# Performance work log

Measured on AMD Instinct MI355X. Metric: run time of the kernel, lower is better.

The kernel has to match this reference:

```python
import jax, jax.numpy as jnp
import numpy as np
from jax import lax

B, CIN, IMG, K = 128, 3, 112, 7
C = 1024      # hidden_channels * channel_dilation
HID = 512     # hidden_channels
HW = (IMG // K) ** 2  # 256 patches
EPS = 1e-5


def _prelu(x, a):
    return jnp.where(x > 0, x, a * x)


def _bn(x, g, b):
    # BatchNorm2d with track_running_stats=False: always uses batch stats
    m = x.mean(axis=(0, 2, 3), keepdims=True)
    v = x.var(axis=(0, 2, 3), keepdims=True)
    return (x - m) * lax.rsqrt(v + EPS) * g[None, :, None, None] + b[None, :, None, None]


def setup_inputs() -> dict:
    key = jax.random.key(0)
    ks = jax.random.split(key, 16)
    d = {
        'x':  jax.random.normal(ks[0], (B, CIN, IMG, IMG), jnp.float32),
        'w0': jax.random.normal(ks[1], (C, CIN, K, K), jnp.float32) * 0.05,
        'b0': jax.random.normal(ks[2], (C,), jnp.float32) * 0.01,
        'a0': jnp.full((1,), 0.25, jnp.float32),
    }
    for i in range(1, 4):
        kw, kb = jax.random.split(jax.random.fold_in(key, i))
        d[f'w{i}'] = jax.random.normal(kw, (C, C), jnp.float32) * 0.02
        d[f'b{i}'] = jax.random.normal(kb, (C,), jnp.float32) * 0.01
        d[f'g{i}'] = jnp.ones((C,), jnp.float32)
        d[f'bt{i}'] = jnp.zeros((C,), jnp.float32)
        d[f'p{i}'] = jnp.full((1,), 0.25, jnp.float32)
    d['pos'] = jax.random.normal(ks[3], (1, HW, C), jnp.float32)
    d['am'] = jnp.full((1,), 0.25, jnp.float32)
    d['wm'] = jax.random.normal(ks[4], (HID, C), jnp.float32) * 0.03
    d['bm'] = jax.random.normal(ks[5], (HID,), jnp.float32) * 0.01
    pkeys = jax.random.split(ks[6], B)
    d['perm'] = jax.vmap(lambda k: jax.random.permutation(k, HW))(pkeys).astype(jnp.int32)
    return d


def reference(x, w0, b0, a0,
              w1, b1, g1, bt1, p1,
              w2, b2, g2, bt2, p2,
              w3, b3, g3, bt3, p3,
              pos, am, wm, bm, perm):
    # patch-embed conv: stride = kernel_size -> [B, C, 16, 16]
    h = lax.conv_general_dilated(x, w0, (K, K), 'VALID',
                                 dimension_numbers=('NCHW', 'OIHW', 'NCHW'))
    h = _prelu(h + b0[None, :, None, None], a0)
    for w, b, g, bt, p in ((w1, b1, g1, bt1, p1),
                           (w2, b2, g2, bt2, p2),
                           (w3, b3, g3, bt3, p3)):
        h = jnp.einsum('bchw,dc->bdhw', h, w) + b[None, :, None, None]  # 1x1 conv
        h = _prelu(_bn(h, g, bt), p)
    Bn, Cn, Hn, Wn = h.shape
    enc = h.reshape(Bn, Cn, Hn * Wn).transpose(0, 2, 1)  # [B, HW, C]
    enc = enc + pos                                      # private: add pos embedding
    enc = _prelu(enc, am) @ wm.T + bm                    # mixer -> [B, HW, HID]
    # private: per-sample token permutation (single batched gather)
    return jnp.take_along_axis(enc, perm[:, :, None], axis=1)
```

## Files before the change

kernel.cpp:

```cpp
#include <hip/hip_runtime.h>
#include <hip/hip_bf16.h>
#include <stdint.h>


typedef __attribute__((ext_vector_type(8))) short bf16x8;
typedef __attribute__((ext_vector_type(4))) float f32x4;

__device__ __forceinline__ float bf2f(uint32_t u) {
  union { uint32_t i; float f; } v; v.i = u << 16; return v.f;
}
__device__ __forceinline__ ushort f2bf(float f) {
  union { float f; uint32_t i; } v; v.f = f;
  uint32_t i = v.i;
  return (ushort)((i + 0x7FFFu + ((i >> 16) & 1u)) >> 16);
}

template<int EPI, int XB, int K, int DOUT>
__global__ void __launch_bounds__(512, 2)
gemm_kernel(const ushort* __restrict__ A, const ushort* __restrict__ Bw,
            const float* __restrict__ bias, const float* __restrict__ alpha,
            void* __restrict__ outp, float* __restrict__ part,
            const int* __restrict__ inv)
{
  __shared__ __align__(16) ushort At[2][256 * 64];
  __shared__ __align__(16) ushort Bt[2][256 * 64];
  const int tid  = threadIdx.x;
  const int lane = tid & 63;
  const int wid  = tid >> 6;
  const int wm   = wid >> 2;
  const int wn   = wid & 3;

  const int s = blockIdx.x;
  const int j = s >> 3;
  const int x = j & ((1 << XB) - 1);
  const int y = ((j >> XB) << 3) | (s & 7);
  const int t0 = y << 8;
  const int d0 = x << 8;

  f32x4 acc[8][4] = {};

  const int swz = (((lane >> 4) ^ (lane & 7)) << 4);
  const char* LA0 = (const char*)&At[0][0] + ((((wm << 7) + (lane & 15))) << 7) + swz;
  const char* LA1 = (const char*)&At[0][0] + ((((wm << 7) + (lane & 15))) << 7) + (swz ^ 64);
  const char* LB0 = (const char*)&Bt[0][0] + ((((wn << 6) + (lane & 15))) << 7) + swz;
  const char* LB1 = (const char*)&Bt[0][0] + ((((wn << 6) + (lane & 15))) << 7) + (swz ^ 64);

  const int lrow8 = lane >> 3;
  const int csrc  = (lane & 7) ^ lrow8;
  const ushort* gAw = A  + (size_t)(t0 + (wid << 4) + lrow8) * K + (csrc << 3);
  const ushort* gBw = Bw + (size_t)(d0 + (wid << 4) + lrow8) * K + (csrc << 3);
  char* stA = (char*)&At[0][0] + (wid << 11);
  char* stB = (char*)&Bt[0][0] + (wid << 11);

#define STAGE_A(T, BUF, H) do {                                                          \
    __builtin_amdgcn_global_load_lds(                                                    \
      (const __attribute__((address_space(1))) uint32_t*)(gAw + (size_t)((H)*128)*K + ((size_t)(T) << 6)),     \
      (__attribute__((address_space(3))) uint32_t*)(stA + (BUF)*32768 + (H)*16384), 16, 0, 0);                  \
    __builtin_amdgcn_global_load_lds(                                                    \
      (const __attribute__((address_space(1))) uint32_t*)(gAw + (size_t)((H)*128+8)*K + ((size_t)(T) << 6)),   \
      (__attribute__((address_space(3))) uint32_t*)(stA + (BUF)*32768 + (H)*16384 + 1024), 16, 0, 0);           \
  } while (0)
#define STAGE_B(T, BUF, H) do {                                                          \
    __builtin_amdgcn_global_load_lds(                                                    \
      (const __attribute__((address_space(1))) uint32_t*)(gBw + (size_t)((H)*128)*K + ((size_t)(T) << 6)),     \
      (__attribute__((address_space(3))) uint32_t*)(stB + (BUF)*32768 + (H)*16384), 16, 0, 0);                  \
    __builtin_amdgcn_global_load_lds(                                                    \
      (const __attribute__((address_space(1))) uint32_t*)(gBw + (size_t)((H)*128+8)*K + ((size_t)(T) << 6)),   \
      (__attribute__((address_space(3))) uint32_t*)(stB + (BUF)*32768 + (H)*16384 + 1024), 16, 0, 0);           \
  } while (0)

#define RD_A(dst, BASE, CUR, MH) do {                                                    \
    dst[0] = *(const bf16x8*)((BASE) + (CUR)*32768 + (MH)*8192 + 0);                     \
    dst[1] = *(const bf16x8*)((BASE) + (CUR)*32768 + (MH)*8192 + 2048);                  \
    dst[2] = *(const bf16x8*)((BASE) + (CUR)*32768 + (MH)*8192 + 4096);                  \
    dst[3] = *(const bf16x8*)((BASE) + (CUR)*32768 + (MH)*8192 + 6144);                  \
  } while (0)
#define RD_B(dst, BASE, CUR) do {                                                        \
    dst[0] = *(const bf16x8*)((BASE) + (CUR)*32768 + 0);                                 \
    dst[1] = *(const bf16x8*)((BASE) + (CUR)*32768 + 2048);                              \
    dst[2] = *(const bf16x8*)((BASE) + (CUR)*32768 + 4096);                              \
    dst[3] = *(const bf16x8*)((BASE) + (CUR)*32768 + 6144);                              \
  } while (0)
#define MFMA16(AF, BF, MH) do {                                                          \
    __builtin_amdgcn_s_setprio(1);                                                       \
    _Pragma("unroll")                                                                    \
    for (int m_ = 0; m_ < 4; ++m_)                                                       \
      _Pragma("unroll")                                                                  \
      for (int n_ = 0; n_ < 4; ++n_)                                                     \
        acc[((MH) << 2) + m_][n_] = __builtin_amdgcn_mfma_f32_16x16x32_bf16(             \
            AF[m_], BF[n_], acc[((MH) << 2) + m_][n_], 0, 0, 0);                         \
    __builtin_amdgcn_s_setprio(0);                                                       \
  } while (0)

#define TILE_BODY(T, CUR, HN1, HN2) do {                                                 \
                               \
    if (HN1) { asm volatile("s_waitcnt vmcnt(4)" ::: "memory"); }                        \
    else     { asm volatile("s_waitcnt vmcnt(0)" ::: "memory"); }                        \
    __builtin_amdgcn_s_barrier();                                                        \
                                                                                \
    RD_A(aX, LA0, CUR, 0);                                                               \
    RD_B(b0f, LB0, CUR);                                                                 \
    if (HN1) { STAGE_A((T) + 1, (CUR) ^ 1, 0); STAGE_A((T) + 1, (CUR) ^ 1, 1); }         \
    MFMA16(aX, b0f, 0);                                                                  \
                                                                                \
    RD_A(aY, LA0, CUR, 1);                                                               \
    MFMA16(aY, b0f, 1);                                                                  \
                                                                                \
    RD_A(aX, LA1, CUR, 0);                                                               \
    RD_B(b1f, LB1, CUR);                                                                 \
    MFMA16(aX, b1f, 0);                                                                  \
                       \
    __builtin_amdgcn_s_barrier();                                                        \
    if (HN2) { STAGE_B((T) + 2, CUR, 0); STAGE_B((T) + 2, CUR, 1); }                     \
                                  \
    RD_A(aY, LA1, CUR, 1);                                                               \
    MFMA16(aY, b1f, 1);                                                                  \
  } while (0)

  constexpr int NT = K >> 6;

  STAGE_A(0, 0, 0); STAGE_A(0, 0, 1);
  STAGE_B(0, 0, 0); STAGE_B(0, 0, 1);
  STAGE_B(1, 1, 0); STAGE_B(1, 1, 1);

  bf16x8 aX[4], aY[4], b0f[4], b1f[4];

#pragma unroll 1
  for (int tp = 0; tp < NT; tp += 2) {
    const bool m1 = (tp + 2 < NT);
    TILE_BODY(tp,     0, true, m1);
    TILE_BODY(tp + 1, 1, m1, m1);
  }

  float bs[4];
#pragma unroll
  for (int n = 0; n < 4; ++n) bs[n] = bias[d0 + (wn << 6) + (n << 4) + (lane & 15)];
  float a0v = (EPI == 0) ? alpha[0] : 0.0f;
  float sA[4] = {0.f, 0.f, 0.f, 0.f}, s2A[4] = {0.f, 0.f, 0.f, 0.f};

#pragma unroll
  for (int m = 0; m < 8; ++m) {
#pragma unroll
    for (int r = 0; r < 4; ++r) {
      int row = t0 + (wm << 7) + (m << 4) + ((lane >> 4) << 2) + r;
      int orow = (EPI == 2) ? ((row & ~255) | inv[row]) : row;
#pragma unroll
      for (int n = 0; n < 4; ++n) {
        int d = d0 + (wn << 6) + (n << 4) + (lane & 15);
        float v = acc[m][n][r] + bs[n];
        if (EPI == 0) v = v > 0.f ? v : a0v * v;
        if (EPI == 1) { sA[n] += v; s2A[n] += v * v; }
        if (EPI == 2) ((float*)outp)[(size_t)orow * DOUT + d] = v;
        else          ((ushort*)outp)[(size_t)row * DOUT + d] = f2bf(v);
      }
    }
  }

  if (EPI == 1) {
    float2* sm = (float2*)&At[0][0];
    int slot = (wm << 2) | (lane >> 4);
    __syncthreads();
#pragma unroll
    for (int n = 0; n < 4; ++n) {
      int c = (wn << 6) + (n << 4) + (lane & 15);
      sm[slot * 256 + c] = make_float2(sA[n], s2A[n]);
    }
    __syncthreads();
    if (tid < 256) {
      float ss = 0.f, ss2 = 0.f;
      for (int q = 0; q < 8; ++q) {
        float2 v = sm[q * 256 + tid];
        ss += v.x; ss2 += v.y;
      }
      part[(size_t)y * 2048 + d0 + tid]        = ss;
      part[(size_t)y * 2048 + 1024 + d0 + tid] = ss2;
    }
  }
#undef STAGE_A
#undef STAGE_B
#undef RD_A
#undef RD_B
#undef MFMA16
#undef TILE_BODY
}

__global__ void bnfold_kernel(const float* __restrict__ part, const float* __restrict__ g,
                              const float* __restrict__ bt, float* __restrict__ scsh) {
  int d = (blockIdx.x << 8) + threadIdx.x;
  float s = 0.f, s2 = 0.f;
  for (int j = 0; j < 128; ++j) { s += part[j * 2048 + d]; s2 += part[j * 2048 + 1024 + d]; }
  float mean = s * (1.f / 32768.f);
  float var  = s2 * (1.f / 32768.f) - mean * mean;
  float sc = g[d] * rsqrtf(var + 1e-5f);
  scsh[d] = sc;
  scsh[1024 + d] = bt[d] - mean * sc;
}

template<bool MIX>
__global__ void bnact_kernel(ushort* __restrict__ Y, const float* __restrict__ scsh,
                             const float* __restrict__ p, const float* __restrict__ pos,
                             const float* __restrict__ am) {
  float pp = p[0];
  float aa = MIX ? am[0] : 0.f;
#pragma unroll 1
  for (int it = 0; it < 8; ++it) {
    size_t vi = ((size_t)it << 19) + ((size_t)blockIdx.x << 8) + threadIdx.x;
    size_t i = vi << 3;
    int d = (int)(i & 1023);
    float pv[8];
    if (MIX) {
      int prow = (int)((i >> 10) & 255);
      const float4* pb = (const float4*)(pos + ((size_t)prow << 10) + d);
      float4 pA = pb[0], pB = pb[1];
      pv[0]=pA.x; pv[1]=pA.y; pv[2]=pA.z; pv[3]=pA.w;
      pv[4]=pB.x; pv[5]=pB.y; pv[6]=pB.z; pv[7]=pB.w;
    }
    uint4 raw = *(const uint4*)(Y + i);
    uint32_t w[4] = {raw.x, raw.y, raw.z, raw.w};
    uint32_t o[4];
#pragma unroll
    for (int q = 0; q < 4; ++q) {
      int dd = d + q * 2;
      float v0 = bf2f(w[q] & 0xFFFFu) * scsh[dd]     + scsh[1024 + dd];
      float v1 = bf2f(w[q] >> 16)     * scsh[dd + 1] + scsh[1024 + dd + 1];
      v0 = v0 > 0.f ? v0 : pp * v0;
      v1 = v1 > 0.f ? v1 : pp * v1;
      if (MIX) {
        v0 += pv[2 * q];     v1 += pv[2 * q + 1];
        v0 = v0 > 0.f ? v0 : aa * v0;
        v1 = v1 > 0.f ? v1 : aa * v1;
      }
      o[q] = (uint32_t)f2bf(v0) | ((uint32_t)f2bf(v1) << 16);
    }
    *(uint4*)(Y + i) = make_uint4(o[0], o[1], o[2], o[3]);
  }
}

__global__ void invperm_kernel(const int* __restrict__ perm, int* __restrict__ inv) {
  int t = (blockIdx.x << 8) + threadIdx.x;
  inv[(t & ~255) + perm[t]] = t & 255;
}

__global__ void f2b_all_kernel(const float* __restrict__ w1, const float* __restrict__ w2,
                               const float* __restrict__ w3, const float* __restrict__ wm,
                               ushort* __restrict__ o1, ushort* __restrict__ o2,
                               ushort* __restrict__ o3, ushort* __restrict__ om) {
  int i = (blockIdx.x << 8) + threadIdx.x;
#pragma unroll
  for (int r = 0; r < 2; ++r) {
    int idx = (r << 19) + i;
    o1[idx] = f2bf(w1[idx]);
    o2[idx] = f2bf(w2[idx]);
    o3[idx] = f2bf(w3[idx]);
  }
  om[i] = f2bf(wm[i]);
}

__global__ void padw0_kernel(const float* __restrict__ w0, ushort* __restrict__ o) {
  int d = blockIdx.x, j = threadIdx.x;
  o[d * 256 + j] = (j < 147) ? f2bf(w0[d * 147 + j]) : (ushort)0;
}

__global__ void im2col_kernel(const float* __restrict__ x, ushort* __restrict__ P) {
  int t0 = blockIdx.x << 4;
  int j = threadIdx.x;
#pragma unroll 1
  for (int tt = 0; tt < 16; ++tt) {
    int t = t0 + tt;
    ushort v = 0;
    if (j < 147) {
      int b = t >> 8, pidx = t & 255;
      int pi = pidx >> 4, pj = pidx & 15;
      int cin = j / 49, rem = j - cin * 49;
      int dy = rem / 7, dx = rem - dy * 7;
      v = f2bf(x[(size_t)(b * 3 + cin) * 12544 + (size_t)(pi * 7 + dy) * 112 + (pj * 7 + dx)]);
    }
    P[(size_t)t * 256 + j] = v;
  }
}

extern "C" void kernel_launch(void* const* d_in, const int* in_sizes, int n_in,
                              void* d_out, int out_size, void* d_ws, size_t ws_size,
                              hipStream_t stream) {
  const float* x   = (const float*)d_in[0];
  const float* w0  = (const float*)d_in[1];
  const float* b0  = (const float*)d_in[2];
  const float* a0  = (const float*)d_in[3];
  const float* w1  = (const float*)d_in[4];
  const float* b1  = (const float*)d_in[5];
  const float* g1  = (const float*)d_in[6];
  const float* bt1 = (const float*)d_in[7];
  const float* p1  = (const float*)d_in[8];
  const float* w2  = (const float*)d_in[9];
  const float* b2  = (const float*)d_in[10];
  const float* g2  = (const float*)d_in[11];
  const float* bt2 = (const float*)d_in[12];
  const float* p2  = (const float*)d_in[13];
  const float* w3  = (const float*)d_in[14];
  const float* b3  = (const float*)d_in[15];
  const float* g3  = (const float*)d_in[16];
  const float* bt3 = (const float*)d_in[17];
  const float* p3  = (const float*)d_in[18];
  const float* pos = (const float*)d_in[19];
  const float* am  = (const float*)d_in[20];
  const float* wm  = (const float*)d_in[21];
  const float* bm  = (const float*)d_in[22];
  const int*  perm = (const int*)d_in[23];

  char* ws = (char*)d_ws;
  ushort* B0   = (ushort*)ws;
  ushort* B1   = (ushort*)(ws + 67108864);
  float*  part = (float*)(ws + 134217728);
  float*  scsh = (float*)(ws + 134217728 + 2097152);
  int*    inv  = (int*)  (ws + 134217728 + 2097152 + 8192);
  char*   wb   = ws + 134217728 + 2097152 + 8192 + 131072;
  ushort* w1b  = (ushort*)wb;
  ushort* w2b  = w1b + 1048576;
  ushort* w3b  = w2b + 1048576;
  ushort* wmb  = w3b + 1048576;
  ushort* w0b  = wmb + 524288;

  invperm_kernel<<<dim3(128), dim3(256), 0, stream>>>(perm, inv);
  f2b_all_kernel<<<dim3(2048), dim3(256), 0, stream>>>(w1, w2, w3, wm, w1b, w2b, w3b, wmb);
  padw0_kernel<<<dim3(1024), dim3(256), 0, stream>>>(w0, w0b);
  im2col_kernel<<<dim3(2048), dim3(256), 0, stream>>>(x, B1);

  gemm_kernel<0, 2, 256, 1024><<<dim3(512), dim3(512), 0, stream>>>(
      B1, w0b, b0, a0, (void*)B0, nullptr, nullptr);

  gemm_kernel<1, 2, 1024, 1024><<<dim3(512), dim3(512), 0, stream>>>(
      B0, w1b, b1, nullptr, (void*)B1, part, nullptr);
  bnfold_kernel<<<dim3(4), dim3(256), 0, stream>>>(part, g1, bt1, scsh);
  bnact_kernel<false><<<dim3(2048), dim3(256), 0, stream>>>(B1, scsh, p1, nullptr, nullptr);

  gemm_kernel<1, 2, 1024, 1024><<<dim3(512), dim3(512), 0, stream>>>(
      B1, w2b, b2, nullptr, (void*)B0, part, nullptr);
  bnfold_kernel<<<dim3(4), dim3(256), 0, stream>>>(part, g2, bt2, scsh);
  bnact_kernel<false><<<dim3(2048), dim3(256), 0, stream>>>(B0, scsh, p2, nullptr, nullptr);

  gemm_kernel<1, 2, 1024, 1024><<<dim3(512), dim3(512), 0, stream>>>(
      B0, w3b, b3, nullptr, (void*)B1, part, nullptr);
  bnfold_kernel<<<dim3(4), dim3(256), 0, stream>>>(part, g3, bt3, scsh);
  bnact_kernel<true><<<dim3(2048), dim3(256), 0, stream>>>(B1, scsh, p3, pos, am);

  gemm_kernel<2, 1, 1024, 512><<<dim3(256), dim3(512), 0, stream>>>(
      B1, wmb, bm, nullptr, d_out, nullptr, inv);
}
```

Measured before the change: 399.3 us.

## Reorder GEMM LDS reads around barriers and merge prep kernels into one launch

Inside the GEMM tile body, all B fragments and both A halves are now read from LDS up front, and the second barrier plus the B staging for tile T+2 move to the middle of the tile, before the second MFMA half. This is meant to batch LDS reads ahead of the MFMAs and start the global B prefetch earlier. It raises register pressure, since aX, aY, b0f and b1f are all live at once, which risks spills under launch_bounds(512,2). Separately, the four preprocessing kernels (im2col, weight conversion, inverse permutation, w0 padding) are fused into one block-partitioned launch to cut launch overhead.

After: 396.3 us. No clear change (-0.7%).

```diff
diff --git a/kernel.cpp b/kernel.cpp
--- a/kernel.cpp
+++ b/kernel.cpp
@@ -93,27 +93,25 @@
   } while (0)
 
 #define TILE_BODY(T, CUR, HN1, HN2) do {                                                 \
-                               \
+                         \
     if (HN1) { asm volatile("s_waitcnt vmcnt(4)" ::: "memory"); }                        \
     else     { asm volatile("s_waitcnt vmcnt(0)" ::: "memory"); }                        \
     __builtin_amdgcn_s_barrier();                                                        \
-                                                                                \
+                 \
+    RD_B(b0f, LB0, CUR);                                                                 \
+    RD_B(b1f, LB1, CUR);                                                                 \
     RD_A(aX, LA0, CUR, 0);                                                               \
-    RD_B(b0f, LB0, CUR);                                                                 \
+    RD_A(aY, LA0, CUR, 1);                                                               \
     if (HN1) { STAGE_A((T) + 1, (CUR) ^ 1, 0); STAGE_A((T) + 1, (CUR) ^ 1, 1); }         \
     MFMA16(aX, b0f, 0);                                                                  \
-                                                                                \
-    RD_A(aY, LA0, CUR, 1);                                                               \
     MFMA16(aY, b0f, 1);                                                                  \
-                                                                                \
+                      \
+    __builtin_amdgcn_s_barrier();                                                        \
+                                                                           \
+    if (HN2) { STAGE_B((T) + 2, CUR, 0); STAGE_B((T) + 2, CUR, 1); }                     \
     RD_A(aX, LA1, CUR, 0);                                                               \
-    RD_B(b1f, LB1, CUR);                                                                 \
+    RD_A(aY, LA1, CUR, 1);                                                               \
     MFMA16(aX, b1f, 0);                                                                  \
-                       \
-    __builtin_amdgcn_s_barrier();                                                        \
-    if (HN2) { STAGE_B((T) + 2, CUR, 0); STAGE_B((T) + 2, CUR, 1); }                     \
-                                  \
-    RD_A(aY, LA1, CUR, 1);                                                               \
     MFMA16(aY, b1f, 1);                                                                  \
   } while (0)
 
@@ -236,46 +234,46 @@
   }
 }
 
-__global__ void invperm_kernel(const int* __restrict__ perm, int* __restrict__ inv) {
-  int t = (blockIdx.x << 8) + threadIdx.x;
-  inv[(t & ~255) + perm[t]] = t & 255;
-}
-
-__global__ void f2b_all_kernel(const float* __restrict__ w1, const float* __restrict__ w2,
-                               const float* __restrict__ w3, const float* __restrict__ wm,
-                               ushort* __restrict__ o1, ushort* __restrict__ o2,
-                               ushort* __restrict__ o3, ushort* __restrict__ om) {
-  int i = (blockIdx.x << 8) + threadIdx.x;
-#pragma unroll
-  for (int r = 0; r < 2; ++r) {
-    int idx = (r << 19) + i;
-    o1[idx] = f2bf(w1[idx]);
-    o2[idx] = f2bf(w2[idx]);
-    o3[idx] = f2bf(w3[idx]);
-  }
-  om[i] = f2bf(wm[i]);
-}
-
-__global__ void padw0_kernel(const float* __restrict__ w0, ushort* __restrict__ o) {
-  int d = blockIdx.x, j = threadIdx.x;
-  o[d * 256 + j] = (j < 147) ? f2bf(w0[d * 147 + j]) : (ushort)0;
-}
-
-__global__ void im2col_kernel(const float* __restrict__ x, ushort* __restrict__ P) {
-  int t0 = blockIdx.x << 4;
-  int j = threadIdx.x;
+__global__ void prep_kernel(const float* __restrict__ x,
+                            const float* __restrict__ w0, const float* __restrict__ w1,
+                            const float* __restrict__ w2, const float* __restrict__ w3,
+                            const float* __restrict__ wm, const int* __restrict__ perm,
+                            ushort* __restrict__ P, ushort* __restrict__ w0b,
+                            ushort* __restrict__ w1b, ushort* __restrict__ w2b,
+                            ushort* __restrict__ w3b, ushort* __restrict__ wmb,
+                            int* __restrict__ inv) {
+  const int b = blockIdx.x, tid = threadIdx.x;
+  if (b < 2048) {
+    int t0 = b << 4;
 #pragma unroll 1
-  for (int tt = 0; tt < 16; ++tt) {
-    int t = t0 + tt;
-    ushort v = 0;
-    if (j < 147) {
-      int b = t >> 8, pidx = t & 255;
-      int pi = pidx >> 4, pj = pidx & 15;
-      int cin = j / 49, rem = j - cin * 49;
-      int dy = rem / 7, dx = rem - dy * 7;
-      v = f2bf(x[(size_t)(b * 3 + cin) * 12544 + (size_t)(pi * 7 + dy) * 112 + (pj * 7 + dx)]);
-    }
-    P[(size_t)t * 256 + j] = v;
+    for (int tt = 0; tt < 16; ++tt) {
+      int t = t0 + tt;
+      ushort v = 0;
+      if (tid < 147) {
+        int bb = t >> 8, pidx = t & 255;
+        int pi = pidx >> 4, pj = pidx & 15;
+        int cin = tid / 49, rem = tid - cin * 49;
+        int dy = rem / 7, dx = rem - dy * 7;
+        v = f2bf(x[(size_t)(bb * 3 + cin) * 12544 + (size_t)(pi * 7 + dy) * 112 + (pj * 7 + dx)]);
+      }
+      P[(size_t)t * 256 + tid] = v;
+    }
+  } else if (b < 4096) {
+    int i = ((b - 2048) << 8) + tid;
+#pragma unroll
+    for (int r = 0; r < 2; ++r) {
+      int idx = (r << 19) + i;
+      w1b[idx] = f2bf(w1[idx]);
+      w2b[idx] = f2bf(w2[idx]);
+      w3b[idx] = f2bf(w3[idx]);
+    }
+    wmb[i] = f2bf(wm[i]);
+  } else if (b < 4224) {
+    int t = ((b - 4096) << 8) + tid;
+    inv[(t & ~255) + perm[t]] = t & 255;
+  } else {
+    int d = b - 4224;
+    w0b[d * 256 + tid] = (tid < 147) ? f2bf(w0[d * 147 + tid]) : (ushort)0;
   }
 }
 
@@ -320,10 +318,8 @@
   ushort* wmb  = w3b + 1048576;
   ushort* w0b  = wmb + 524288;
 
-  invperm_kernel<<<dim3(128), dim3(256), 0, stream>>>(perm, inv);
-  f2b_all_kernel<<<dim3(2048), dim3(256), 0, stream>>>(w1, w2, w3, wm, w1b, w2b, w3b, wmb);
-  padw0_kernel<<<dim3(1024), dim3(256), 0, stream>>>(w0, w0b);
-  im2col_kernel<<<dim3(2048), dim3(256), 0, stream>>>(x, B1);
+  prep_kernel<<<dim3(5248), dim3(256), 0, stream>>>(
+      x, w0, w1, w2, w3, wm, perm, B1, w0b, w1b, w2b, w3b, wmb, inv);
 
   gemm_kernel<0, 2, 256, 1024><<<dim3(512), dim3(512), 0, stream>>>(
       B1, w0b, b0, a0, (void*)B0, nullptr, nullptr);
```
